# Performance work log

Measured on AMD Instinct MI355X. Metric: run time of the kernel, lower is better.

Reference implementation:

```python
import jax, jax.numpy as jnp
import numpy as np

N, C, H, W = 32, 256, 64, 64
STRIDE = 4  # slices of refs' H dim per block, as in the torch mem_save path
EPS = 1e-12  # F.normalize clamp_min eps


def setup_inputs() -> dict:
    key = jax.random.key(0)
    k1, k2 = jax.random.split(key)
    refs = jax.random.normal(k1, (N, C, H, W), dtype=jnp.float32)
    img = jax.random.normal(k2, (C, H, W), dtype=jnp.float32)
    return {"refs": refs, "img": img}


def _l2_normalize(x, axis):
    # matches torch.nn.functional.normalize(p=2): x / max(||x||, eps)
    n = jnp.sqrt(jnp.sum(x * x, axis=axis, keepdims=True))
    return x / jnp.maximum(n, EPS)


def reference(refs, img):
    # refs: (N, C, H, W), img: (C, H, W)
    refs_n = _l2_normalize(refs, axis=1)
    img_n = _l2_normalize(img, axis=0)

    img_flat = img_n.reshape(C, H * W).T  # (HW, C) query vectors

    # group reference feature vectors by blocks of STRIDE rows of refs' H dim:
    # (N,C,H,W) -> (H, N, W, C) -> (H//STRIDE, STRIDE*N*W, C)
    blocks = refs_n.transpose(2, 0, 3, 1).reshape(H // STRIDE, STRIDE * N * W, C)

    def step(running_max, block):
        # (HW, C) x (blocksize, C)^T -> (HW, blocksize) cosine sims
        sim = jnp.einsum('xc,yc->xy', img_flat, block)
        return jnp.maximum(running_max, sim.max(axis=1)), None

    init = jnp.full((H * W,), -jnp.inf, dtype=img_flat.dtype)
    best, _ = jax.lax.scan(step, init, blocks)
    return best.reshape(H, W)
```

## Files before the change

kernel.cpp:

```cpp
#include <hip/hip_runtime.h>

#define CN 256
#define HN 64
#define WN 64
#define NNW 32
#define HW (HN*WN)
#define NREF (NNW*HW)
#define KD 256

#define BM2 128
#define BN2 128
#define NCH 32
#define NTILES (NREF/NCH/BN2)

using bf16x8 = __attribute__((ext_vector_type(8))) short;
using f32x4  = __attribute__((ext_vector_type(4))) float;

__device__ inline unsigned short f2bf(float x) {
  unsigned int u = __float_as_uint(x);
  return (unsigned short)((u + 0x7fffu + ((u >> 16) & 1u)) >> 16);
}

__device__ inline void atomicMaxFloat(float* addr, float val) {
  if (val >= 0.f) atomicMax(reinterpret_cast<int*>(addr), __float_as_int(val));
  else            atomicMin(reinterpret_cast<unsigned int*>(addr), __float_as_uint(val));
}

__device__ inline void gload_lds16(const void* g, void* l) {
  __builtin_amdgcn_global_load_lds(
      (const __attribute__((address_space(1))) void*)g,
      (__attribute__((address_space(3))) void*)l, 16, 0, 0);
}

__global__ __launch_bounds__(256)
void norm_kernel(const float* __restrict__ refs, const float* __restrict__ img,
                 unsigned short* __restrict__ Rb, unsigned short* __restrict__ Qb,
                 float* __restrict__ out) {
  __shared__ float tile[CN][WN + 1];
  __shared__ float ssq[4][WN];
  __shared__ float scl[WN];
  const int bid = blockIdx.x;
  const int t = threadIdx.x;
  const float* src; unsigned short* dst; int nh;
  if (bid < NNW * HN) { src = refs; dst = Rb; nh = bid; }
  else {
    src = img; dst = Qb; nh = bid - NNW * HN;
    if (t < 64) out[(size_t)nh * 64 + t] = -INFINITY;
  }
  const float* base = src + (size_t)(nh >> 6) * (CN * (size_t)HW) + (size_t)(nh & 63) * WN;

  const int c16 = t >> 4, w4 = (t & 15) * 4;
#pragma unroll
  for (int j = 0; j < 16; ++j) {
    int c = j * 16 + c16;
    float4 v = *(const float4*)&base[(size_t)c * HW + w4];
    tile[c][w4 + 0] = v.x; tile[c][w4 + 1] = v.y;
    tile[c][w4 + 2] = v.z; tile[c][w4 + 3] = v.w;
  }
  __syncthreads();
  {
    int w = t & 63, vv = t >> 6;
    float s = 0.f;
#pragma unroll 8
    for (int cc = 0; cc < 64; ++cc) { float x = tile[vv * 64 + cc][w]; s += x * x; }
    ssq[vv][w] = s;
  }
  __syncthreads();
  if (t < 64)
    scl[t] = 1.f / fmaxf(sqrtf(ssq[0][t] + ssq[1][t] + ssq[2][t] + ssq[3][t]), 1e-12f);
  __syncthreads();
  const int w = t >> 2, cq = t & 3;
  unsigned short* orow = dst + ((size_t)nh * WN + w) * KD;
  const float sc = scl[w];
#pragma unroll
  for (int j = 0; j < 8; ++j) {
    int c0 = (j * 4 + cq) * 8;
    bf16x8 o;
#pragma unroll
    for (int k = 0; k < 8; ++k) o[k] = (short)f2bf(tile[c0 + k][w] * sc);
    *(bf16x8*)&orow[c0] = o;
  }
}

#define BARR() __builtin_amdgcn_s_barrier()
#define SCHED0() __builtin_amdgcn_sched_barrier(0)
#define GATE(N) asm volatile("s_waitcnt vmcnt(" #N ")" ::: "memory")
#define LGKM0() asm volatile("s_waitcnt lgkmcnt(0)" ::: "memory")

#define STG4(SUB, PTR, KOFF) do { \
  _Pragma("unroll") \
  for (int p = 0; p < 4; ++p) \
    gload_lds16((PTR) + (KOFF) + p * 8 * KD, &lds[SUB][(w * 32 + p * 8) * 64]); \
} while (0)

#define PH(CSUB, ACM, DOSTG, SSUB, KOFF, GN) do { \
  if (DOSTG) STG4(SSUB, rs, KOFF); \
  GATE(GN); BARR(); SCHED0(); \
  bf16x8 bb[2][4]; \
  _Pragma("unroll") \
  for (int ks = 0; ks < 2; ++ks) \
  _Pragma("unroll") \
  for (int ni = 0; ni < 4; ++ni) \
    bb[ks][ni] = *(const bf16x8*)&lds[CSUB][(nrow + ni * 16) * 64 + (ks ? (pk0 ^ 32) : pk0)]; \
  __builtin_amdgcn_s_setprio(1); \
  _Pragma("unroll") \
  for (int ks = 0; ks < 2; ++ks) \
  _Pragma("unroll") \
  for (int mi = 0; mi < 4; ++mi) \
  _Pragma("unroll") \
  for (int ni = 0; ni < 4; ++ni) \
    acc[mi][ni] = __builtin_amdgcn_mfma_f32_16x16x32_bf16(a[mi][(CSUB)*2 + ks], bb[ks][ni], ((ACM) || ks) ? acc[mi][ni] : ZZ, 0, 0, 0); \
  __builtin_amdgcn_s_setprio(0); \
  SCHED0(); BARR(); \
} while (0)

#define FOLD() do { \
  _Pragma("unroll") \
  for (int mi = 0; mi < 4; ++mi) \
  _Pragma("unroll") \
  for (int ee = 0; ee < 4; ++ee) { \
    float v0 = fmaxf(acc[mi][0][ee], acc[mi][1][ee]); \
    float v1 = fmaxf(acc[mi][2][ee], acc[mi][3][ee]); \
    run[mi][ee] = fmaxf(run[mi][ee], fmaxf(v0, v1)); \
  } \
} while (0)

__global__ __launch_bounds__(256, 2)
void simmax_kernel(const unsigned short* __restrict__ Q,
                   const unsigned short* __restrict__ R,
                   float* __restrict__ out) {
  __shared__ unsigned short lds[4][8192];

  const int t = threadIdx.x;
  const int lane = t & 63;
  const int w  = t >> 6;
  const int wm = w >> 1;
  const int wn = w & 1;

  const int wg  = (blockIdx.x & 7) * 128 + (blockIdx.x >> 3);
  const int nch = wg >> 5;
  const int bm  = wg & 31;

  const int srow = lane >> 3;
  const int schunk = (lane & 7) ^ srow;
  const unsigned short* qsrcA = Q + (size_t)(bm * BM2 + w * 32 + srow) * KD + schunk * 8;
  const unsigned short* rsrc0 = R + (size_t)((size_t)nch * (NTILES * BN2) + w * 32 + srow) * KD + schunk * 8;

  const int pk0 = (((lane >> 4) ^ (lane & 7))) * 8;
  const int mrow = wm * 64 + (lane & 15);
  const int nrow = wn * 64 + (lane & 15);

  const f32x4 ZZ = {0.f, 0.f, 0.f, 0.f};
  f32x4 acc[4][4];
  f32x4 run[4];
#pragma unroll
  for (int mi = 0; mi < 4; ++mi)
#pragma unroll
    for (int ee = 0; ee < 4; ++ee) run[mi][ee] = -1e30f;

#pragma unroll
  for (int s = 0; s < 4; ++s)
    STG4(s, qsrcA, s * 64);
  GATE(0); BARR(); SCHED0();

  bf16x8 a[4][8];
#pragma unroll
  for (int mi = 0; mi < 4; ++mi) {
    const int rb = (mrow + mi * 16) * 64;
#pragma unroll
    for (int kq = 0; kq < 4; ++kq) {
      a[mi][kq * 2 + 0] = *(const bf16x8*)&lds[kq][rb + pk0];
      a[mi][kq * 2 + 1] = *(const bf16x8*)&lds[kq][rb + (pk0 ^ 32)];
    }
  }
  LGKM0(); BARR();

  const unsigned short* rs = rsrc0;
  STG4(0, rs, 0);
  STG4(1, rs, 64);
  STG4(2, rs, 128);

  for (int bt = 0; bt < NTILES - 1; ++bt) {
    PH(0,  0,  1,  3,  192,            12);
    PH(1,  1,  1,  0,  32768,          12);
    PH(2,  1,  1,  1,  32768 + 64,     12);
    PH(3,  1,  1,  2,  32768 + 128,    12);
    FOLD();
    rs += 32768;
  }
  PH(0, 0, 1, 3, 192, 12);
  PH(1, 1, 0, 0, 0,    8);
  PH(2, 1, 0, 0, 0,    4);
  PH(3, 1, 0, 0, 0,    0);
  FOLD();

#pragma unroll
  for (int mi = 0; mi < 4; ++mi)
#pragma unroll
  for (int ee = 0; ee < 4; ++ee) {
    float v = run[mi][ee];
    v = fmaxf(v, __shfl_xor(v, 1));
    v = fmaxf(v, __shfl_xor(v, 2));
    v = fmaxf(v, __shfl_xor(v, 4));
    v = fmaxf(v, __shfl_xor(v, 8));
    if ((lane & 15) == 0)
      atomicMaxFloat(&out[bm * BM2 + wm * 64 + mi * 16 + (lane >> 4) * 4 + ee], v);
  }
}

extern "C" void kernel_launch(void* const* d_in, const int* in_sizes, int n_in,
                              void* d_out, int out_size, void* d_ws, size_t ws_size,
                              hipStream_t stream) {
  const float* refs = (const float*)d_in[0];
  const float* img  = (const float*)d_in[1];
  float* out = (float*)d_out;

  unsigned short* Rb = (unsigned short*)d_ws;
  unsigned short* Qb = Rb + (size_t)NREF * KD;

  hipLaunchKernelGGL(norm_kernel, dim3(NNW * HN + HN), dim3(256), 0, stream,
                     refs, img, Rb, Qb, out);
  hipLaunchKernelGGL(simmax_kernel, dim3(NCH * (HW / BM2)), dim3(256), 0, stream,
                     Qb, Rb, out);
}
```

Baseline: 247.1 us.

## Switch simmax to 32x32x16 MFMA with paired K-stage pipeline and fewer chunks

Replaces the 16x16x32 bf16 MFMA tiling with 32x32x16 MFMAs, giving each wave 2x2 accumulators of 16 floats. The K loop now runs two phases, each covering two LDS stages, instead of four. It also halves the number of reference chunks so each block processes more tiles, and adjusts the output shuffle-reduction and row mapping for the new accumulator layout. The aim is to cut LDS B-fragment reads per FLOP and barrier count, plus fewer atomics. The trade-off is larger register use and fewer blocks in the grid.

After: 262.2 us. 1.06x slower.

```diff
diff --git a/kernel.cpp b/kernel.cpp
--- a/kernel.cpp
+++ b/kernel.cpp
@@ -10,11 +10,11 @@
 
 #define BM2 128
 #define BN2 128
-#define NCH 32
+#define NCH 16
 #define NTILES (NREF/NCH/BN2)
 
 using bf16x8 = __attribute__((ext_vector_type(8))) short;
-using f32x4  = __attribute__((ext_vector_type(4))) float;
+using f32x16 = __attribute__((ext_vector_type(16))) float;
 
 __device__ inline unsigned short f2bf(float x) {
   unsigned int u = __float_as_uint(x);
@@ -93,36 +93,33 @@
     gload_lds16((PTR) + (KOFF) + p * 8 * KD, &lds[SUB][(w * 32 + p * 8) * 64]); \
 } while (0)
 
-#define PH(CSUB, ACM, DOSTG, SSUB, KOFF, GN) do { \
-  if (DOSTG) STG4(SSUB, rs, KOFF); \
+#define PH2(PAIR, ACM, STGM, GN) do { \
+  if ((STGM) == 1) { STG4(2, rs, 128); STG4(3, rs, 192); } \
+  if ((STGM) == 2) { STG4(0, rs + 32768, 0); STG4(1, rs + 32768, 64); } \
   GATE(GN); BARR(); SCHED0(); \
-  bf16x8 bb[2][4]; \
-  _Pragma("unroll") \
-  for (int ks = 0; ks < 2; ++ks) \
-  _Pragma("unroll") \
-  for (int ni = 0; ni < 4; ++ni) \
-    bb[ks][ni] = *(const bf16x8*)&lds[CSUB][(nrow + ni * 16) * 64 + (ks ? (pk0 ^ 32) : pk0)]; \
   __builtin_amdgcn_s_setprio(1); \
   _Pragma("unroll") \
-  for (int ks = 0; ks < 2; ++ks) \
-  _Pragma("unroll") \
-  for (int mi = 0; mi < 4; ++mi) \
-  _Pragma("unroll") \
-  for (int ni = 0; ni < 4; ++ni) \
-    acc[mi][ni] = __builtin_amdgcn_mfma_f32_16x16x32_bf16(a[mi][(CSUB)*2 + ks], bb[ks][ni], ((ACM) || ks) ? acc[mi][ni] : ZZ, 0, 0, 0); \
+  for (int kf = 0; kf < 8; ++kf) { \
+    const int sub = (PAIR) * 2 + (kf >> 2); \
+    const int ck = ((((kf & 3) * 2 + hi) ^ l7)) * 8; \
+    bf16x8 b0 = *(const bf16x8*)&lds[sub][nrowb * 64 + ck]; \
+    bf16x8 b1 = *(const bf16x8*)&lds[sub][(nrowb + 32) * 64 + ck]; \
+    _Pragma("unroll") \
+    for (int mi = 0; mi < 2; ++mi) { \
+      acc[mi][0] = __builtin_amdgcn_mfma_f32_32x32x16_bf16(a[mi][(PAIR)*8 + kf], b0, ((ACM) || kf) ? acc[mi][0] : ZZ, 0, 0, 0); \
+      acc[mi][1] = __builtin_amdgcn_mfma_f32_32x32x16_bf16(a[mi][(PAIR)*8 + kf], b1, ((ACM) || kf) ? acc[mi][1] : ZZ, 0, 0, 0); \
+    } \
+  } \
   __builtin_amdgcn_s_setprio(0); \
   SCHED0(); BARR(); \
 } while (0)
 
 #define FOLD() do { \
   _Pragma("unroll") \
-  for (int mi = 0; mi < 4; ++mi) \
-  _Pragma("unroll") \
-  for (int ee = 0; ee < 4; ++ee) { \
-    float v0 = fmaxf(acc[mi][0][ee], acc[mi][1][ee]); \
-    float v1 = fmaxf(acc[mi][2][ee], acc[mi][3][ee]); \
-    run[mi][ee] = fmaxf(run[mi][ee], fmaxf(v0, v1)); \
-  } \
+  for (int mi = 0; mi < 2; ++mi) \
+  _Pragma("unroll") \
+  for (int e = 0; e < 16; ++e) \
+    run[mi][e] = fmaxf(run[mi][e], fmaxf(acc[mi][0][e], acc[mi][1][e])); \
 } while (0)
 
 __global__ __launch_bounds__(256, 2)
@@ -136,8 +133,10 @@
   const int w  = t >> 6;
   const int wm = w >> 1;
   const int wn = w & 1;
-
-  const int wg  = (blockIdx.x & 7) * 128 + (blockIdx.x >> 3);
+  const int hi = lane >> 5;
+  const int l7 = lane & 7;
+
+  const int wg  = (blockIdx.x & 7) * 64 + (blockIdx.x >> 3);
   const int nch = wg >> 5;
   const int bm  = wg & 31;
 
@@ -146,65 +145,59 @@
   const unsigned short* qsrcA = Q + (size_t)(bm * BM2 + w * 32 + srow) * KD + schunk * 8;
   const unsigned short* rsrc0 = R + (size_t)((size_t)nch * (NTILES * BN2) + w * 32 + srow) * KD + schunk * 8;
 
-  const int pk0 = (((lane >> 4) ^ (lane & 7))) * 8;
-  const int mrow = wm * 64 + (lane & 15);
-  const int nrow = wn * 64 + (lane & 15);
-
-  const f32x4 ZZ = {0.f, 0.f, 0.f, 0.f};
-  f32x4 acc[4][4];
-  f32x4 run[4];
-#pragma unroll
-  for (int mi = 0; mi < 4; ++mi)
-#pragma unroll
-    for (int ee = 0; ee < 4; ++ee) run[mi][ee] = -1e30f;
+  const int mrowb = wm * 64 + (lane & 31);
+  const int nrowb = wn * 64 + (lane & 31);
+
+  const f32x16 ZZ = {0,0,0,0,0,0,0,0,0,0,0,0,0,0,0,0};
+  f32x16 acc[2][2];
+  f32x16 run[2];
+#pragma unroll
+  for (int mi = 0; mi < 2; ++mi)
+#pragma unroll
+    for (int e = 0; e < 16; ++e) run[mi][e] = -1e30f;
 
 #pragma unroll
   for (int s = 0; s < 4; ++s)
     STG4(s, qsrcA, s * 64);
   GATE(0); BARR(); SCHED0();
 
-  bf16x8 a[4][8];
-#pragma unroll
-  for (int mi = 0; mi < 4; ++mi) {
-    const int rb = (mrow + mi * 16) * 64;
-#pragma unroll
-    for (int kq = 0; kq < 4; ++kq) {
-      a[mi][kq * 2 + 0] = *(const bf16x8*)&lds[kq][rb + pk0];
-      a[mi][kq * 2 + 1] = *(const bf16x8*)&lds[kq][rb + (pk0 ^ 32)];
-    }
+  bf16x8 a[2][16];
+#pragma unroll
+  for (int mi = 0; mi < 2; ++mi) {
+    const int rb = (mrowb + mi * 32) * 64;
+#pragma unroll
+    for (int kf = 0; kf < 16; ++kf)
+      a[mi][kf] = *(const bf16x8*)&lds[kf >> 2][rb + ((((kf & 3) * 2 + hi) ^ l7)) * 8];
   }
   LGKM0(); BARR();
 
   const unsigned short* rs = rsrc0;
-  STG4(0, rs, 0);
-  STG4(1, rs, 64);
-  STG4(2, rs, 128);
+  STG4(0, rs, 0); STG4(1, rs, 64);
 
   for (int bt = 0; bt < NTILES - 1; ++bt) {
-    PH(0,  0,  1,  3,  192,            12);
-    PH(1,  1,  1,  0,  32768,          12);
-    PH(2,  1,  1,  1,  32768 + 64,     12);
-    PH(3,  1,  1,  2,  32768 + 128,    12);
+    PH2(0, 0, 1, 8);
+    PH2(1, 1, 2, 8);
     FOLD();
     rs += 32768;
   }
-  PH(0, 0, 1, 3, 192, 12);
-  PH(1, 1, 0, 0, 0,    8);
-  PH(2, 1, 0, 0, 0,    4);
-  PH(3, 1, 0, 0, 0,    0);
+  PH2(0, 0, 1, 8);
+  PH2(1, 1, 0, 0);
   FOLD();
 
 #pragma unroll
-  for (int mi = 0; mi < 4; ++mi)
-#pragma unroll
-  for (int ee = 0; ee < 4; ++ee) {
-    float v = run[mi][ee];
+  for (int mi = 0; mi < 2; ++mi)
+#pragma unroll
+  for (int e = 0; e < 16; ++e) {
+    float v = run[mi][e];
     v = fmaxf(v, __shfl_xor(v, 1));
     v = fmaxf(v, __shfl_xor(v, 2));
     v = fmaxf(v, __shfl_xor(v, 4));
     v = fmaxf(v, __shfl_xor(v, 8));
-    if ((lane & 15) == 0)
-      atomicMaxFloat(&out[bm * BM2 + wm * 64 + mi * 16 + (lane >> 4) * 4 + ee], v);
+    v = fmaxf(v, __shfl_xor(v, 16));
+    if ((lane & 31) == 0) {
+      int row = bm * BM2 + wm * 64 + mi * 32 + (e & 3) + 8 * (e >> 2) + 4 * hi;
+      atomicMaxFloat(&out[row], v);
+    }
   }
 }
 
```

## Halve ref chunk count and pipeline two K-slices per barrier phase

Applied to the files above, without the earlier changes.

The reference set is now split into 16 chunks instead of 32, so each workgroup loops over twice as many tiles and the grid is half as large, with fewer atomic max writes at the end. The software pipeline now stages two 64-wide K sub-slices per phase and computes two sub-slices between barriers, so each tile takes two barrier pairs instead of four. The aim is to cut barrier and wait overhead and amortize the setup of the A operand over more tiles. In exchange there is less prefetch lookahead per phase, and the smaller grid may give poorer load balance across CUs.

Measured after the change: 254.2 us. 1.03x slower.

```diff
diff --git a/kernel.cpp b/kernel.cpp
--- a/kernel.cpp
+++ b/kernel.cpp
@@ -10,7 +10,7 @@
 
 #define BM2 128
 #define BN2 128
-#define NCH 32
+#define NCH 16
 #define NTILES (NREF/NCH/BN2)
 
 using bf16x8 = __attribute__((ext_vector_type(8))) short;
@@ -93,24 +93,31 @@
     gload_lds16((PTR) + (KOFF) + p * 8 * KD, &lds[SUB][(w * 32 + p * 8) * 64]); \
 } while (0)
 
-#define PH(CSUB, ACM, DOSTG, SSUB, KOFF, GN) do { \
-  if (DOSTG) STG4(SSUB, rs, KOFF); \
+#define HALF(SUB, J, ACM0) do { \
+  bf16x8 bb[2][4]; \
+  _Pragma("unroll") \
+  for (int ks = 0; ks < 2; ++ks) \
+  _Pragma("unroll") \
+  for (int ni = 0; ni < 4; ++ni) \
+    bb[ks][ni] = *(const bf16x8*)&lds[SUB][(nrow + ni * 16) * 64 + (ks ? (pk0 ^ 32) : pk0)]; \
+  __builtin_amdgcn_s_setprio(1); \
+  _Pragma("unroll") \
+  for (int ks = 0; ks < 2; ++ks) \
+  _Pragma("unroll") \
+  for (int mi = 0; mi < 4; ++mi) \
+  _Pragma("unroll") \
+  for (int ni = 0; ni < 4; ++ni) \
+    acc[mi][ni] = __builtin_amdgcn_mfma_f32_16x16x32_bf16(a[mi][(SUB)*2 + ks], bb[ks][ni], \
+                      ((ACM0) || (J) || ks) ? acc[mi][ni] : ZZ, 0, 0, 0); \
+  __builtin_amdgcn_s_setprio(0); \
+} while (0)
+
+#define PH(PAIR, ACM0, STGM, GN) do { \
+  if ((STGM) == 1) { STG4(2, rs, 128); STG4(3, rs, 192); } \
+  if ((STGM) == 2) { STG4(0, rs + 32768, 0); STG4(1, rs + 32768, 64); } \
   GATE(GN); BARR(); SCHED0(); \
-  bf16x8 bb[2][4]; \
-  _Pragma("unroll") \
-  for (int ks = 0; ks < 2; ++ks) \
-  _Pragma("unroll") \
-  for (int ni = 0; ni < 4; ++ni) \
-    bb[ks][ni] = *(const bf16x8*)&lds[CSUB][(nrow + ni * 16) * 64 + (ks ? (pk0 ^ 32) : pk0)]; \
-  __builtin_amdgcn_s_setprio(1); \
-  _Pragma("unroll") \
-  for (int ks = 0; ks < 2; ++ks) \
-  _Pragma("unroll") \
-  for (int mi = 0; mi < 4; ++mi) \
-  _Pragma("unroll") \
-  for (int ni = 0; ni < 4; ++ni) \
-    acc[mi][ni] = __builtin_amdgcn_mfma_f32_16x16x32_bf16(a[mi][(CSUB)*2 + ks], bb[ks][ni], ((ACM) || ks) ? acc[mi][ni] : ZZ, 0, 0, 0); \
-  __builtin_amdgcn_s_setprio(0); \
+  HALF((PAIR)*2,     0, ACM0); \
+  HALF((PAIR)*2 + 1, 1, ACM0); \
   SCHED0(); BARR(); \
 } while (0)
 
@@ -137,7 +144,7 @@
   const int wm = w >> 1;
   const int wn = w & 1;
 
-  const int wg  = (blockIdx.x & 7) * 128 + (blockIdx.x >> 3);
+  const int wg  = (blockIdx.x & 7) * 64 + (blockIdx.x >> 3);
   const int nch = wg >> 5;
   const int bm  = wg & 31;
 
@@ -176,22 +183,16 @@
   LGKM0(); BARR();
 
   const unsigned short* rs = rsrc0;
-  STG4(0, rs, 0);
-  STG4(1, rs, 64);
-  STG4(2, rs, 128);
+  STG4(0, rs, 0); STG4(1, rs, 64);
 
   for (int bt = 0; bt < NTILES - 1; ++bt) {
-    PH(0,  0,  1,  3,  192,            12);
-    PH(1,  1,  1,  0,  32768,          12);
-    PH(2,  1,  1,  1,  32768 + 64,     12);
-    PH(3,  1,  1,  2,  32768 + 128,    12);
+    PH(0, 0, 1, 8);
+    PH(1, 1, 2, 8);
     FOLD();
     rs += 32768;
   }
-  PH(0, 0, 1, 3, 192, 12);
-  PH(1, 1, 0, 0, 0,    8);
-  PH(2, 1, 0, 0, 0,    4);
-  PH(3, 1, 0, 0, 0,    0);
+  PH(0, 0, 1, 8);
+  PH(1, 1, 0, 0);
   FOLD();
 
 #pragma unroll
```
